# Kernel tuning notes

Hardware: AMD Instinct MI355X
Metric: run time of the kernel (lower is better)

## Reference

```python
import jax, jax.numpy as jnp
import numpy as np

IN_FEATURES = 256
OUT_FEATURES = 256
INTERNAL = (IN_FEATURES + OUT_FEATURES) // 2  # trajectron AdditiveAttention default


def setup_inputs() -> dict:
    key = jax.random.key(0)
    k1, k2, k3, k4, k5 = jax.random.split(key, 5)
    B, TH, TQ = 32, 256, 64
    inputs = jax.random.normal(k1, (B, TH, IN_FEATURES), dtype=jnp.float32)
    state = jax.random.normal(k2, (B, TQ, OUT_FEATURES), dtype=jnp.float32)
    # Linear weights (no bias), Kaiming-ish scale
    w1 = jax.random.normal(k3, (INTERNAL, IN_FEATURES), dtype=jnp.float32) / np.sqrt(IN_FEATURES)
    w2 = jax.random.normal(k4, (INTERNAL, OUT_FEATURES), dtype=jnp.float32) / np.sqrt(OUT_FEATURES)
    v = jax.random.normal(k5, (INTERNAL,), dtype=jnp.float32) / np.sqrt(INTERNAL)
    return {"inputs": inputs, "state": state, "w1": w1, "w2": w2, "v": v, "batch_size": B}


def reference(inputs, state, w1, w2, v, batch_size):
    # history annotations: (B, Th, Din); future annotations (queries): (B, Tq, Dout)
    keys = inputs.reshape(batch_size, -1, IN_FEATURES)
    queries = state.reshape(batch_size, -1, OUT_FEATURES)
    # Additive (Bahdanau) attention: score = v . tanh(W1 k + W2 q)
    k_proj = jnp.einsum('bti,di->btd', keys, w1)       # (B, Th, D)
    q_proj = jnp.einsum('bqo,do->bqd', queries, w2)    # (B, Tq, D)
    scores = jnp.einsum('d,bqtd->bqt', v, jnp.tanh(q_proj[:, :, None, :] + k_proj[:, None, :, :]))
    alpha = jax.nn.softmax(scores, axis=-1)            # softmax over history axis
    contexts = jnp.einsum('bqt,bti->bqi', alpha, keys)  # (B, Tq, Din)
    # reshape + dropout (eval mode / p effectively 0 -> identity)
    return contexts.reshape(-1, IN_FEATURES)
```

## Files before the change

### kernel.cpp

```cpp
#include <hip/hip_runtime.h>
#include <math.h>

#define BATCH 32
#define TH    256
#define TQn   64
#define DIN   256
#define DD    256
#define QT    8
#define E2C   2.885390081777927f
#define NL2E  -2.8853900817779268f

typedef __attribute__((ext_vector_type(8)))  short bf16x8;
typedef __attribute__((ext_vector_type(16))) float floatx16;
typedef __attribute__((ext_vector_type(4)))  float f32x4;

__device__ __forceinline__ float eclamp(float x) {
    return __builtin_amdgcn_exp2f(fminf(x * E2C, 30.f));
}

__device__ __forceinline__ void split2(float x0, float x1, unsigned& hi, unsigned& lo) {
    unsigned u0 = __float_as_uint(x0), u1 = __float_as_uint(x1);
    unsigned h0 = u0 & 0xFFFF0000u,   h1 = u1 & 0xFFFF0000u;
    float r0 = x0 - __uint_as_float(h0);
    float r1 = x1 - __uint_as_float(h1);
    hi = (u0 >> 16) | h1;
    lo = (__float_as_uint(r0) >> 16) | (__float_as_uint(r1) & 0xFFFF0000u);
}

__device__ __forceinline__ void split8(float4 f0, float4 f1, uint4& hi, uint4& lo) {
    split2(f0.x, f0.y, hi.x, lo.x);
    split2(f0.z, f0.w, hi.y, lo.y);
    split2(f1.x, f1.y, hi.z, lo.z);
    split2(f1.z, f1.w, hi.w, lo.w);
}

#define REG4  65
#define WOFF  (16 * REG4)
#define TSTR  68
__global__ __launch_bounds__(256, 4)
void proj_kernel(const float* __restrict__ keys,
                 const float* __restrict__ state,
                 const float* __restrict__ w1,
                 const float* __restrict__ w2,
                 float* __restrict__ ktp,
                 float* __restrict__ qpo)
{
    __shared__ uint4 lds4[2 * 16 * REG4];

    const int bid = blockIdx.x;
    const int tid = threadIdx.x;

    const float* X;
    const float* W;
    int m0, n0;
    bool is_kp;
    if (bid < 512) {
        is_kp = true;
        m0 = (bid >> 2) * 64;
        n0 = (bid & 3) * 64;
        X = keys; W = w1;
    } else {
        is_kp = false;
        int lb = bid - 512;
        m0 = (lb >> 2) * 64;
        n0 = (lb & 3) * 64;
        X = state; W = w2;
    }

    const int w    = tid >> 6;
    const int l    = tid & 63;
    const int mt   = w >> 1;
    const int nt   = w & 1;
    const int srow = tid >> 3;
    const int kg   = tid & 7;
    const int s_s  = kg >> 1;
    const int lidx = (srow & 31) + 32 * (kg & 1);

    floatx16 acc = {};

    for (int k0 = 0; k0 < DIN; k0 += 64) {
        #pragma unroll
        for (int hrow = 0; hrow < 2; hrow++) {
            int m = srow + hrow * 32;
            const float* px = X + (size_t)(m0 + m) * DIN + k0 + kg * 8;
            uint4 hi, lo;
            split8(*(const float4*)px, *(const float4*)(px + 4), hi, lo);
            int g = m >> 5;
            lds4[((0 * 2 + g) * 4 + s_s) * REG4 + lidx] = hi;
            lds4[((2 + g) * 4 + s_s) * REG4 + lidx] = lo;
            const float* pw = W + (size_t)(n0 + m) * DIN + k0 + kg * 8;
            split8(*(const float4*)pw, *(const float4*)(pw + 4), hi, lo);
            lds4[WOFF + ((0 * 2 + g) * 4 + s_s) * REG4 + lidx] = hi;
            lds4[WOFF + ((2 + g) * 4 + s_s) * REG4 + lidx] = lo;
        }
        __syncthreads();

        #pragma unroll
        for (int s = 0; s < 4; s++) {
            uint4 ahr = lds4[((0 * 2 + mt) * 4 + s) * REG4 + l];
            uint4 alr = lds4[((2 + mt) * 4 + s) * REG4 + l];
            uint4 bhr = lds4[WOFF + ((0 * 2 + nt) * 4 + s) * REG4 + l];
            uint4 blr = lds4[WOFF + ((2 + nt) * 4 + s) * REG4 + l];
            bf16x8 ah = __builtin_bit_cast(bf16x8, ahr);
            bf16x8 al = __builtin_bit_cast(bf16x8, alr);
            bf16x8 bh = __builtin_bit_cast(bf16x8, bhr);
            bf16x8 bl = __builtin_bit_cast(bf16x8, blr);
            acc = __builtin_amdgcn_mfma_f32_32x32x16_bf16(ah, bh, acc, 0, 0, 0);
            acc = __builtin_amdgcn_mfma_f32_32x32x16_bf16(al, bh, acc, 0, 0, 0);
            acc = __builtin_amdgcn_mfma_f32_32x32x16_bf16(ah, bl, acc, 0, 0, 0);
        }
        __syncthreads();
    }

    const int col = l & 31;
    const int hl  = l >> 5;
    if (is_kp) {
        float* sT = (float*)lds4;
        const int d_local = nt * 32 + col;
        #pragma unroll
        for (int r = 0; r < 16; r++) {
            int t_local = mt * 32 + 4 * hl + 8 * (r >> 2) + (r & 3);
            sT[t_local * TSTR + d_local] = eclamp(acc[r]);
        }
        __syncthreads();
        const int b  = m0 >> 8;
        const int t0 = m0 & 255;
        float4* dst4 = (float4*)ktp;
        #pragma unroll
        for (int p = 0; p < 4; p++) {
            int dp_local = w * 4 + p;
            float4 v4 = *(float4*)&sT[l * TSTR + dp_local * 4];
            dst4[(size_t)(b * 64 + (n0 >> 2) + dp_local) * 256 + t0 + l] = v4;
        }
    } else {
        const int d = n0 + nt * 32 + col;
        #pragma unroll
        for (int r = 0; r < 16; r++) {
            int row = (r & 3) + 8 * (r >> 2) + 4 * hl;
            qpo[(size_t)(m0 + mt * 32 + row) * DD + d] = eclamp(acc[r]);
        }
    }
}

__global__ __launch_bounds__(1024, 4)
void attn_kernel(const float* __restrict__ keys,
                 const float* __restrict__ vvec,
                 const float* __restrict__ ktp,
                 const float* __restrict__ qp,
                 float* __restrict__ out)
{
    __shared__ float s_part[4][QT][TH];
    __shared__ float s_alpha[QT][TH];
    __shared__ float s_rsum[QT];

    const int bid  = blockIdx.x;
    const int b    = bid & 31;
    const int q0   = (bid >> 5) * QT;
    const int tid  = threadIdx.x;
    const int t    = tid & 255;
    const int dgu  = __builtin_amdgcn_readfirstlane(tid >> 8);
    const int lane = tid & 63;
    const int wv   = tid >> 6;

    float acc[QT];
    #pragma unroll
    for (int q = 0; q < QT; q++) acc[q] = 0.f;

    const float4* kb4 = (const float4*)ktp + ((size_t)(b * 64 + dgu * 16) * 256 + t);
    const float*  pqb = qp + (size_t)(b * TQn + q0) * DD + dgu * 64;
    const float*  vvp = vvec + dgu * 64;

    float4 kv0 = kb4[0 * 256], kv1 = kb4[1 * 256],
           kv2 = kb4[2 * 256], kv3 = kb4[3 * 256];

    #pragma unroll
    for (int c = 0; c < 4; c++) {
        float4 n0v, n1v, n2v, n3v;
        if (c < 3) {
            const float4* p = kb4 + (size_t)(c + 1) * 4 * 256;
            n0v = p[0 * 256]; n1v = p[1 * 256];
            n2v = p[2 * 256]; n3v = p[3 * 256];
        }
        #pragma unroll
        for (int u = 0; u < 4; u++) {
            const int dp = c * 4 + u;
            float4 kv = (u == 0) ? kv0 : (u == 1) ? kv1 : (u == 2) ? kv2 : kv3;
            const float v0 = vvp[dp * 4 + 0], v1 = vvp[dp * 4 + 1];
            const float v2 = vvp[dp * 4 + 2], v3 = vvp[dp * 4 + 3];
            #pragma unroll
            for (int q = 0; q < QT; q++) {
                const float* pr = pqb + q * DD + dp * 4;
                float d0 = fmaf(pr[0], kv.x, 1.f);
                float d1 = fmaf(pr[1], kv.y, 1.f);
                float n01 = fmaf(v1, d0, v0 * d1);
                acc[q] = fmaf(n01, __builtin_amdgcn_rcpf(d0 * d1), acc[q]);
                float d2 = fmaf(pr[2], kv.z, 1.f);
                float d3 = fmaf(pr[3], kv.w, 1.f);
                float n23 = fmaf(v3, d2, v2 * d3);
                acc[q] = fmaf(n23, __builtin_amdgcn_rcpf(d2 * d3), acc[q]);
            }
        }
        if (c < 3) { kv0 = n0v; kv1 = n1v; kv2 = n2v; kv3 = n3v; }
    }

    #pragma unroll
    for (int q = 0; q < QT; q++) s_part[dgu][q][t] = acc[q];
    __syncthreads();

    if (wv < QT) {
        const int q = wv;
        float p0 = s_part[0][q][lane]       + s_part[1][q][lane]
                 + s_part[2][q][lane]       + s_part[3][q][lane];
        float p1 = s_part[0][q][lane + 64]  + s_part[1][q][lane + 64]
                 + s_part[2][q][lane + 64]  + s_part[3][q][lane + 64];
        float p2 = s_part[0][q][lane + 128] + s_part[1][q][lane + 128]
                 + s_part[2][q][lane + 128] + s_part[3][q][lane + 128];
        float p3 = s_part[0][q][lane + 192] + s_part[1][q][lane + 192]
                 + s_part[2][q][lane + 192] + s_part[3][q][lane + 192];
        float e0 = __builtin_amdgcn_exp2f(p0 * NL2E);
        float e1 = __builtin_amdgcn_exp2f(p1 * NL2E);
        float e2 = __builtin_amdgcn_exp2f(p2 * NL2E);
        float e3 = __builtin_amdgcn_exp2f(p3 * NL2E);
        s_alpha[q][lane]       = e0;
        s_alpha[q][lane + 64]  = e1;
        s_alpha[q][lane + 128] = e2;
        s_alpha[q][lane + 192] = e3;
        float s = (e0 + e1) + (e2 + e3);
        #pragma unroll
        for (int off = 32; off >= 1; off >>= 1) s += __shfl_xor(s, off);
        if (lane == 0) s_rsum[q] = 1.f / s;
    }
    __syncthreads();

    {
        const int iqg = __builtin_amdgcn_readfirstlane((tid >> 6) & 3);
        const int il  = lane & 15;
        const int tl  = lane >> 4;
        const int iq  = iqg * 16 + il;

        f32x4 ctx4[QT] = {};
        const float* kp0 = keys + ((size_t)b * TH + dgu * 64 + tl) * DIN + iq * 4;

        #pragma unroll 4
        for (int step = 0; step < 16; step++) {
            f32x4 key4 = *(const f32x4*)(kp0 + (size_t)step * 4 * DIN);
            const int ta = dgu * 64 + step * 4 + tl;
            #pragma unroll
            for (int q = 0; q < QT; q++)
                ctx4[q] += key4 * s_alpha[q][ta];
        }

        #pragma unroll
        for (int q = 0; q < QT; q++) {
            #pragma unroll
            for (int k = 0; k < 4; k++) {
                ctx4[q][k] += __shfl_xor(ctx4[q][k], 16);
                ctx4[q][k] += __shfl_xor(ctx4[q][k], 32);
            }
        }
        if (tl == 0) {
            #pragma unroll
            for (int q = 0; q < QT; q++)
                *(f32x4*)&s_part[dgu][q][iq * 4] = ctx4[q];
        }
    }
    __syncthreads();

    if (tid < 512) {
        const int q = tid >> 6, iqf = tid & 63;
        f32x4 s = *(const f32x4*)&s_part[0][q][iqf * 4];
        s += *(const f32x4*)&s_part[1][q][iqf * 4];
        s += *(const f32x4*)&s_part[2][q][iqf * 4];
        s += *(const f32x4*)&s_part[3][q][iqf * 4];
        s *= s_rsum[q];
        *(f32x4*)&out[(size_t)(b * TQn + q0 + q) * DIN + iqf * 4] = s;
    }
}

extern "C" void kernel_launch(void* const* d_in, const int* in_sizes, int n_in,
                              void* d_out, int out_size, void* d_ws, size_t ws_size,
                              hipStream_t stream) {
    (void)in_sizes; (void)n_in; (void)out_size; (void)ws_size;
    const float* keys  = (const float*)d_in[0];
    const float* state = (const float*)d_in[1];
    const float* w1    = (const float*)d_in[2];
    const float* w2    = (const float*)d_in[3];
    const float* v     = (const float*)d_in[4];
    float* out = (float*)d_out;

    float* ktp = (float*)d_ws;
    float* qp  = ktp + (size_t)BATCH * DD * TH;

    hipLaunchKernelGGL(proj_kernel, dim3(640), dim3(256), 0, stream,
                       keys, state, w1, w2, ktp, qp);
    hipLaunchKernelGGL(attn_kernel, dim3(BATCH * (TQn / QT)), dim3(1024), 0, stream,
                       keys, v, ktp, qp, out);
}
```

Measured before the change: 107.5 us.

## Halve queries per block, preload key projections, cache alpha in registers

Cuts the number of queries handled per block from 8 to 4, which doubles the block count and spreads the score work over more CUs. All 16 key-projection float4 loads are now issued up front instead of being double-buffered in chunks. The context pass gives each lane 16 contiguous history steps and reads their alpha values from LDS as vectors into registers. The final store is now a per-thread scalar write. Each block now re-reads the same keys for fewer queries, and register pressure rises from holding the loaded vectors.

```diff
diff --git a/kernel.cpp b/kernel.cpp
--- a/kernel.cpp
+++ b/kernel.cpp
@@ -6,7 +6,7 @@
 #define TQn   64
 #define DIN   256
 #define DD    256
-#define QT    8
+#define QT    4
 #define E2C   2.885390081777927f
 #define NL2E  -2.8853900817779268f
 
@@ -170,37 +170,27 @@
     const float*  pqb = qp + (size_t)(b * TQn + q0) * DD + dgu * 64;
     const float*  vvp = vvec + dgu * 64;
 
-    float4 kv0 = kb4[0 * 256], kv1 = kb4[1 * 256],
-           kv2 = kb4[2 * 256], kv3 = kb4[3 * 256];
-
-    #pragma unroll
-    for (int c = 0; c < 4; c++) {
-        float4 n0v, n1v, n2v, n3v;
-        if (c < 3) {
-            const float4* p = kb4 + (size_t)(c + 1) * 4 * 256;
-            n0v = p[0 * 256]; n1v = p[1 * 256];
-            n2v = p[2 * 256]; n3v = p[3 * 256];
-        }
-        #pragma unroll
-        for (int u = 0; u < 4; u++) {
-            const int dp = c * 4 + u;
-            float4 kv = (u == 0) ? kv0 : (u == 1) ? kv1 : (u == 2) ? kv2 : kv3;
-            const float v0 = vvp[dp * 4 + 0], v1 = vvp[dp * 4 + 1];
-            const float v2 = vvp[dp * 4 + 2], v3 = vvp[dp * 4 + 3];
-            #pragma unroll
-            for (int q = 0; q < QT; q++) {
-                const float* pr = pqb + q * DD + dp * 4;
-                float d0 = fmaf(pr[0], kv.x, 1.f);
-                float d1 = fmaf(pr[1], kv.y, 1.f);
-                float n01 = fmaf(v1, d0, v0 * d1);
-                acc[q] = fmaf(n01, __builtin_amdgcn_rcpf(d0 * d1), acc[q]);
-                float d2 = fmaf(pr[2], kv.z, 1.f);
-                float d3 = fmaf(pr[3], kv.w, 1.f);
-                float n23 = fmaf(v3, d2, v2 * d3);
-                acc[q] = fmaf(n23, __builtin_amdgcn_rcpf(d2 * d3), acc[q]);
-            }
-        }
-        if (c < 3) { kv0 = n0v; kv1 = n1v; kv2 = n2v; kv3 = n3v; }
+    float4 kvv[16];
+    #pragma unroll
+    for (int dp = 0; dp < 16; dp++) kvv[dp] = kb4[(size_t)dp * 256];
+
+    #pragma unroll
+    for (int dp = 0; dp < 16; dp++) {
+        const float4 kv = kvv[dp];
+        const float v0 = vvp[dp * 4 + 0], v1 = vvp[dp * 4 + 1];
+        const float v2 = vvp[dp * 4 + 2], v3 = vvp[dp * 4 + 3];
+        #pragma unroll
+        for (int q = 0; q < QT; q++) {
+            const float* pr = pqb + q * DD + dp * 4;
+            float d0 = fmaf(pr[0], kv.x, 1.f);
+            float d1 = fmaf(pr[1], kv.y, 1.f);
+            float n01 = fmaf(v1, d0, v0 * d1);
+            acc[q] = fmaf(n01, __builtin_amdgcn_rcpf(d0 * d1), acc[q]);
+            float d2 = fmaf(pr[2], kv.z, 1.f);
+            float d3 = fmaf(pr[3], kv.w, 1.f);
+            float n23 = fmaf(v3, d2, v2 * d3);
+            acc[q] = fmaf(n23, __builtin_amdgcn_rcpf(d2 * d3), acc[q]);
+        }
     }
 
     #pragma unroll
@@ -237,17 +227,24 @@
         const int il  = lane & 15;
         const int tl  = lane >> 4;
         const int iq  = iqg * 16 + il;
+        const int tbase = dgu * 64 + tl * 16;
+
+        f32x4 al[QT][4];
+        #pragma unroll
+        for (int q = 0; q < QT; q++)
+            #pragma unroll
+            for (int c = 0; c < 4; c++)
+                al[q][c] = *(const f32x4*)&s_alpha[q][tbase + c * 4];
 
         f32x4 ctx4[QT] = {};
-        const float* kp0 = keys + ((size_t)b * TH + dgu * 64 + tl) * DIN + iq * 4;
-
-        #pragma unroll 4
+        const float* kp0 = keys + ((size_t)b * TH + tbase) * DIN + iq * 4;
+
+        #pragma unroll
         for (int step = 0; step < 16; step++) {
-            f32x4 key4 = *(const f32x4*)(kp0 + (size_t)step * 4 * DIN);
-            const int ta = dgu * 64 + step * 4 + tl;
+            f32x4 key4 = *(const f32x4*)(kp0 + (size_t)step * DIN);
             #pragma unroll
             for (int q = 0; q < QT; q++)
-                ctx4[q] += key4 * s_alpha[q][ta];
+                ctx4[q] += key4 * al[q][step >> 2][step & 3];
         }
 
         #pragma unroll
@@ -266,14 +263,11 @@
     }
     __syncthreads();
 
-    if (tid < 512) {
-        const int q = tid >> 6, iqf = tid & 63;
-        f32x4 s = *(const f32x4*)&s_part[0][q][iqf * 4];
-        s += *(const f32x4*)&s_part[1][q][iqf * 4];
-        s += *(const f32x4*)&s_part[2][q][iqf * 4];
-        s += *(const f32x4*)&s_part[3][q][iqf * 4];
-        s *= s_rsum[q];
-        *(f32x4*)&out[(size_t)(b * TQn + q0 + q) * DIN + iqf * 4] = s;
+    {
+        const int q = tid >> 8, ii = tid & 255;
+        float s = s_part[0][q][ii] + s_part[1][q][ii]
+                + s_part[2][q][ii] + s_part[3][q][ii];
+        out[(size_t)(b * TQn + q0 + q) * DIN + ii] = s * s_rsum[q];
     }
 }
 
```

After: 109.0 us. About the same (+1.4%).
